# Kernel tuning notes

Measured on AMD Instinct MI355X. Metric: run time of the kernel, lower is better.

## Reference

```python
import jax, jax.numpy as jnp
import numpy as np

D_MODEL = 1024
NUM_HEADS = 16
HEAD_DIM = D_MODEL // NUM_HEADS
HIDDEN = 4096
EPS = 1e-10


def _layernorm(x, gamma, beta):
    mean = jnp.mean(x, axis=-1, keepdims=True)
    var = jnp.var(x, axis=-1, keepdims=True)  # unbiased=False
    return gamma * (x - mean) / jnp.sqrt(var + EPS) + beta


def setup_inputs() -> dict:
    key = jax.random.key(0)
    ks = jax.random.split(key, 16)
    s = 0.02
    d, h = D_MODEL, HIDDEN
    inp = {
        "x": jax.random.normal(ks[0], (4, 2048, d), dtype=jnp.float32),
        "Wq": jax.random.normal(ks[1], (d, d), dtype=jnp.float32) * s,
        "bq": jnp.zeros((d,), jnp.float32),
        "Wk": jax.random.normal(ks[2], (d, d), dtype=jnp.float32) * s,
        "bk": jnp.zeros((d,), jnp.float32),
        "Wv": jax.random.normal(ks[3], (d, d), dtype=jnp.float32) * s,
        "bv": jnp.zeros((d,), jnp.float32),
        "Wo": jax.random.normal(ks[4], (d, d), dtype=jnp.float32) * s,
        "bo": jnp.zeros((d,), jnp.float32),
        "W1": jax.random.normal(ks[5], (d, h), dtype=jnp.float32) * s,
        "b1": jnp.zeros((h,), jnp.float32),
        "W2": jax.random.normal(ks[6], (h, d), dtype=jnp.float32) * s,
        "b2": jnp.zeros((d,), jnp.float32),
        "gamma1": jnp.ones((d,), jnp.float32),
        "beta1": jnp.zeros((d,), jnp.float32),
        "gamma2": jnp.ones((d,), jnp.float32),
        "beta2": jnp.zeros((d,), jnp.float32),
    }
    return inp


def reference(x, Wq, bq, Wk, bk, Wv, bv, Wo, bo, W1, b1, W2, b2,
              gamma1, beta1, gamma2, beta2):
    B, S, D = x.shape
    H, hd = NUM_HEADS, HEAD_DIM
    scale = jnp.sqrt(jnp.float32(hd))

    # --- sublayer 1: self-attention on norm(x), residual add ---
    xn = _layernorm(x, gamma1, beta1)
    Q = (xn @ Wq + bq).reshape(B, S, H, hd).transpose(0, 2, 1, 3)  # [B,H,S,hd]
    K = (xn @ Wk + bk).reshape(B, S, H, hd).transpose(0, 2, 1, 3)
    V = (xn @ Wv + bv).reshape(B, S, H, hd).transpose(0, 2, 1, 3)
    scores = jnp.einsum("bhqd,bhkd->bhqk", Q, K) / scale  # [B,H,S,S]
    attn = jax.nn.softmax(scores, axis=-1)
    ctx = jnp.einsum("bhqk,bhkd->bhqd", attn, V)  # [B,H,S,hd]
    ctx = ctx.transpose(0, 2, 1, 3).reshape(B, S, D)
    x = x + (ctx @ Wo + bo)

    # --- sublayer 2: FFN on norm(x), residual add ---
    xn = _layernorm(x, gamma2, beta2)
    h = jax.nn.gelu(xn @ W1 + b1, approximate=False)  # torch F.gelu default = erf
    x = x + (h @ W2 + b2)
    return x
```

## Files before the change

### kernel.cpp

```cpp
#include <hip/hip_runtime.h>
#include <stdint.h>

#define D_MODEL 1024
#define HIDDEN  4096
#define SEQ     2048
#define NTOK    8192
#define NHEAD   16
#define HDIM    64

typedef unsigned short u16;
typedef __attribute__((ext_vector_type(8))) __bf16 bf16x8;
typedef __attribute__((ext_vector_type(4))) float f32x4;

__device__ __forceinline__ u16 f2bf(float f) {
  union { float f; unsigned u; } c; c.f = f;
  unsigned u = c.u + 0x7fffu + ((c.u >> 16) & 1u);
  return (u16)(u >> 16);
}

__device__ __forceinline__ void gload16(const void* g, void* l) {
  __builtin_amdgcn_global_load_lds((const __attribute__((address_space(1))) void*)g,
                                   (__attribute__((address_space(3))) void*)l, 16, 0, 0);
}

__global__ void transpose_cvt(const float* __restrict__ W, u16* __restrict__ Wt, int K, int N) {
  __shared__ float t[32][33];
  const int k0 = blockIdx.y * 32, n0 = blockIdx.x * 32;
  const int tx = threadIdx.x, ty = threadIdx.y;
#pragma unroll
  for (int p = 0; p < 4; ++p)
    t[ty + p * 8][tx] = W[(size_t)(k0 + ty + p * 8) * N + n0 + tx];
  __syncthreads();
#pragma unroll
  for (int p = 0; p < 4; ++p) {
    const int n = ty + p * 8;
    Wt[(size_t)(n0 + n) * K + k0 + tx] = f2bf(t[tx][n]);
  }
}

__global__ __launch_bounds__(256)
void ln_kernel(const float* __restrict__ x, const float* __restrict__ gamma,
               const float* __restrict__ beta, u16* __restrict__ out) {
  const int row = blockIdx.x;
  const int tid = threadIdx.x;
  const float4 v = ((const float4*)(x + (size_t)row * D_MODEL))[tid];
  float s = v.x + v.y + v.z + v.w;
  float q = v.x * v.x + v.y * v.y + v.z * v.z + v.w * v.w;
#pragma unroll
  for (int o = 32; o > 0; o >>= 1) { s += __shfl_down(s, o); q += __shfl_down(q, o); }
  __shared__ float ps[4], pq[4];
  const int wid = tid >> 6, lane = tid & 63;
  if (lane == 0) { ps[wid] = s; pq[wid] = q; }
  __syncthreads();
  s = ps[0] + ps[1] + ps[2] + ps[3];
  q = pq[0] + pq[1] + pq[2] + pq[3];
  const float mean = s * (1.0f / D_MODEL);
  const float var = q * (1.0f / D_MODEL) - mean * mean;
  const float rstd = rsqrtf(var + 1e-10f);
  const float4 gv = ((const float4*)gamma)[tid];
  const float4 bv = ((const float4*)beta)[tid];
  ushort4 o4;
  o4.x = f2bf((v.x - mean) * rstd * gv.x + bv.x);
  o4.y = f2bf((v.y - mean) * rstd * gv.y + bv.y);
  o4.z = f2bf((v.z - mean) * rstd * gv.z + bv.z);
  o4.w = f2bf((v.w - mean) * rstd * gv.w + bv.w);
  ((ushort4*)(out + (size_t)row * D_MODEL))[tid] = o4;
}

#define SLOT_AE (256 * 32)
#define SLOT_BE (128 * 32)
#define SLOT_E  (SLOT_AE + SLOT_BE)
#define SLOT_BYTES (SLOT_E * 2)

template <int EPI, int KPY, int KPX>
__global__ __launch_bounds__(512, 4)
void gemm32(const u16* __restrict__ A, const u16* __restrict__ Bt,
            const float* __restrict__ bias, const float* __restrict__ res,
            void* __restrict__ outp, int M, int N, int K) {
  __shared__ u16 Ls[3 * SLOT_E];
  const int tid = threadIdx.x;
  const int wid = tid >> 6, lane = tid & 63;
  const int g = lane >> 4, lr = lane & 15;
  const int wr = wid >> 1, wc = wid & 1;

  const int xcd = blockIdx.x & 7, l = blockIdx.x >> 3;
  int bx, by;
  if (KPY > 0) { by = xcd * KPY + (l % KPY); bx = l / KPY; }
  else         { bx = xcd * KPX + (l % KPX); by = l / KPX; }
  const int m0 = by * 256, n0 = bx * 128;

  const int NT = K >> 5;

  const int rA0 = tid >> 2, cc0 = ((tid & 3) ^ (rA0 & 3)) << 3;
  const int u1 = tid + 512;
  const int rA1 = u1 >> 2, cc1 = (((u1 & 3) ^ (rA1 & 3))) << 3;
  const u16* pA0 = A + (size_t)(m0 + rA0) * K + cc0;
  const u16* pA1 = A + (size_t)(m0 + rA1) * K + cc1;
  const u16* pB0 = Bt + (size_t)(n0 + rA0) * K + cc0;
  const int dA0 = wid * 1024;
  const int dA1 = wid * 1024 + 8192;
  const int dB0 = SLOT_AE * 2 + wid * 1024;

  auto stage = [&](int slot) {
    char* sb = (char*)Ls + slot * SLOT_BYTES;
    gload16(pA0, sb + dA0);
    gload16(pA1, sb + dA1);
    gload16(pB0, sb + dB0);
    pA0 += 32; pA1 += 32; pB0 += 32;
  };

  stage(0); stage(1); stage(2);

  f32x4 acc[4][4] = {};
  const int cx = (g ^ (lr & 3)) << 3;

  for (int t = 0; t < NT; ++t) {
    if (t + 3 <= NT)      asm volatile("s_waitcnt vmcnt(6)" ::: "memory");
    else if (t + 2 <= NT) asm volatile("s_waitcnt vmcnt(3)" ::: "memory");
    else                  asm volatile("s_waitcnt vmcnt(0)" ::: "memory");
    asm volatile("s_barrier" ::: "memory");

    const int slot = t % 3;
    const u16* sA = Ls + slot * SLOT_E;
    const u16* sB = sA + SLOT_AE;
    bf16x8 af[4], bfr[4];
#pragma unroll
    for (int mf = 0; mf < 4; ++mf)
      af[mf] = *(const bf16x8*)(sA + (wr * 64 + mf * 16 + lr) * 32 + cx);
#pragma unroll
    for (int nf = 0; nf < 4; ++nf)
      bfr[nf] = *(const bf16x8*)(sB + (wc * 64 + nf * 16 + lr) * 32 + cx);

    __builtin_amdgcn_s_setprio(1);
#pragma unroll
    for (int mf = 0; mf < 4; ++mf)
#pragma unroll
      for (int nf = 0; nf < 4; ++nf)
        acc[mf][nf] = __builtin_amdgcn_mfma_f32_16x16x32_bf16(af[mf], bfr[nf], acc[mf][nf], 0, 0, 0);
    __builtin_amdgcn_s_setprio(0);

    if (t + 3 < NT) {
      asm volatile("s_barrier" ::: "memory");
      stage(slot);
    }
  }

#pragma unroll
  for (int mf = 0; mf < 4; ++mf)
#pragma unroll
    for (int nf = 0; nf < 4; ++nf) {
      const int gn = n0 + wc * 64 + nf * 16 + lr;
      const int gm = m0 + wr * 64 + mf * 16 + 4 * g;
      const float bv = (EPI == 3) ? 0.f : bias[gn];
      const int gn_p = (EPI == 3) ? ((gn & ~63) | ((gn & 15) << 2) | ((gn >> 4) & 3)) : gn;
#pragma unroll
      for (int r = 0; r < 4; ++r) {
        const size_t idx = (size_t)(gm + r) * N + gn_p;
        if (EPI == 0) {
          ((u16*)outp)[idx] = f2bf(acc[mf][nf][r] + bv);
        } else if (EPI == 1) {
          ((float*)outp)[idx] = acc[mf][nf][r] + bv + res[idx];
        } else if (EPI == 2) {
          const float v = acc[mf][nf][r] + bv;
          ((u16*)outp)[idx] = f2bf(0.5f * v * (1.0f + erff(v * 0.7071067811865475f)));
        } else if (EPI == 3) {
          ((u16*)outp)[idx] = f2bf(acc[mf][nf][r] + bias[gm + r]);
        } else {
          ((u16*)outp)[idx] = f2bf((acc[mf][nf][r] + bv) * 0.125f);
        }
      }
    }
}

__global__ __launch_bounds__(256, 4)
void attn_kernel(const u16* __restrict__ Q, const u16* __restrict__ K,
                 const u16* __restrict__ Vt, u16* __restrict__ ctxo) {
  const int bh = blockIdx.y;
  const int b = bh >> 4, h = bh & 15;
  const int q0 = blockIdx.x * 128;
  const int tid = threadIdx.x, wid = tid >> 6, lane = tid & 63;
  const int g = lane >> 4, lr = lane & 15;
  const size_t base = ((size_t)b * SEQ) * D_MODEL + h * HDIM;
  const size_t vbase = ((size_t)h * HDIM) * NTOK + (size_t)b * SEQ;

  __shared__ u16 Ks[64 * 72];
  __shared__ u16 Vts[64 * 72];
  __shared__ u16 Ps[128 * 72];

  const int qw = wid * 32;

#pragma unroll
  for (int i = 0; i < 4; ++i) {
    const int ch = tid + 256 * i, row = ch >> 3, j = ch & 7;
    *(bf16x8*)(Ps + row * 72 + j * 8) =
        *(const bf16x8*)(Q + base + (size_t)(q0 + row) * D_MODEL + j * 8);
  }
  __syncthreads();
  bf16x8 aq[2][2];
#pragma unroll
  for (int qf = 0; qf < 2; ++qf)
#pragma unroll
    for (int ks = 0; ks < 2; ++ks)
      aq[qf][ks] = *(const bf16x8*)(Ps + (qw + qf * 16 + lr) * 72 + ks * 32 + g * 8);

  f32x4 o[2][4] = {};
  float lrun[2][4] = {};

  for (int kv0 = 0; kv0 < SEQ; kv0 += 64) {
    __syncthreads();
#pragma unroll
    for (int i = 0; i < 2; ++i) {
      const int row = (tid >> 3) + i * 32, j = tid & 7;
      *(bf16x8*)(Ks + row * 72 + j * 8) =
          *(const bf16x8*)(K + base + (size_t)(kv0 + row) * D_MODEL + j * 8);
      *(bf16x8*)(Vts + row * 72 + j * 8) =
          *(const bf16x8*)(Vt + vbase + (size_t)row * NTOK + kv0 + j * 8);
    }
    __syncthreads();

    f32x4 s[2][4] = {};
    __builtin_amdgcn_s_setprio(1);
#pragma unroll
    for (int ks = 0; ks < 2; ++ks)
#pragma unroll
      for (int kf = 0; kf < 4; ++kf) {
        const bf16x8 bk = *(const bf16x8*)(Ks + (kf * 16 + lr) * 72 + ks * 32 + g * 8);
#pragma unroll
        for (int qf = 0; qf < 2; ++qf)
          s[qf][kf] = __builtin_amdgcn_mfma_f32_16x16x32_bf16(aq[qf][ks], bk, s[qf][kf], 0, 0, 0);
      }
    __builtin_amdgcn_s_setprio(0);

#pragma unroll
    for (int qf = 0; qf < 2; ++qf)
#pragma unroll
      for (int r = 0; r < 4; ++r) {
        union { float f; unsigned u; } p0, p1, p2, p3;
        p0.f = __expf(s[qf][0][r]);
        p1.f = __expf(s[qf][1][r]);
        p2.f = __expf(s[qf][2][r]);
        p3.f = __expf(s[qf][3][r]);
        lrun[qf][r] += (p0.f + p1.f) + (p2.f + p3.f);
        const unsigned lo = __builtin_amdgcn_perm(p1.u + 0x8000u, p0.u + 0x8000u, 0x07060302u);
        const unsigned hi = __builtin_amdgcn_perm(p3.u + 0x8000u, p2.u + 0x8000u, 0x07060302u);
        *(uint2*)(Ps + (qw + qf * 16 + 4 * g + r) * 72 + lr * 4) = make_uint2(lo, hi);
      }
    asm volatile("s_waitcnt lgkmcnt(0)" ::: "memory");

    __builtin_amdgcn_s_setprio(1);
#pragma unroll
    for (int ks = 0; ks < 2; ++ks) {
      bf16x8 pf[2];
#pragma unroll
      for (int qf = 0; qf < 2; ++qf)
        pf[qf] = *(const bf16x8*)(Ps + (qw + qf * 16 + lr) * 72 + ks * 32 + g * 8);
#pragma unroll
      for (int df = 0; df < 4; ++df) {
        const bf16x8 vf = *(const bf16x8*)(Vts + (df * 16 + lr) * 72 + ks * 32 + g * 8);
#pragma unroll
        for (int qf = 0; qf < 2; ++qf)
          o[qf][df] = __builtin_amdgcn_mfma_f32_16x16x32_bf16(pf[qf], vf, o[qf][df], 0, 0, 0);
      }
    }
    __builtin_amdgcn_s_setprio(0);
  }

#pragma unroll
  for (int off = 1; off < 16; off <<= 1)
#pragma unroll
    for (int qf = 0; qf < 2; ++qf)
#pragma unroll
      for (int r = 0; r < 4; ++r)
        lrun[qf][r] += __shfl_xor(lrun[qf][r], off);

#pragma unroll
  for (int qf = 0; qf < 2; ++qf)
#pragma unroll
    for (int r = 0; r < 4; ++r) {
      const float rinv = 1.0f / lrun[qf][r];
      const int qrow = q0 + qw + qf * 16 + 4 * g + r;
#pragma unroll
      for (int df = 0; df < 4; ++df)
        ctxo[base + (size_t)qrow * D_MODEL + df * 16 + lr] = f2bf(o[qf][df][r] * rinv);
    }
}

extern "C" void kernel_launch(void* const* d_in, const int* in_sizes, int n_in,
                              void* d_out, int out_size, void* d_ws, size_t ws_size,
                              hipStream_t stream) {
  const float* x  = (const float*)d_in[0];
  const float* Wq = (const float*)d_in[1];
  const float* bq = (const float*)d_in[2];
  const float* Wk = (const float*)d_in[3];
  const float* bk = (const float*)d_in[4];
  const float* Wv = (const float*)d_in[5];
  const float* bv = (const float*)d_in[6];
  const float* Wo = (const float*)d_in[7];
  const float* bo = (const float*)d_in[8];
  const float* W1 = (const float*)d_in[9];
  const float* b1 = (const float*)d_in[10];
  const float* W2 = (const float*)d_in[11];
  const float* b2 = (const float*)d_in[12];
  const float* gamma1 = (const float*)d_in[13];
  const float* beta1  = (const float*)d_in[14];
  const float* gamma2 = (const float*)d_in[15];
  const float* beta2  = (const float*)d_in[16];
  float* out = (float*)d_out;

  const size_t M1 = 1u << 20;
  u16* w   = (u16*)d_ws;
  u16* WtQ = w;
  u16* WtK = w + 1 * M1;
  u16* WtV = w + 2 * M1;
  u16* WtO = w + 3 * M1;
  u16* Wt1 = w + 4 * M1;
  u16* Wt2 = w + 8 * M1;
  u16* xn  = w + 12 * M1;
  u16* Qb  = w + 20 * M1;
  u16* Kb  = w + 28 * M1;
  u16* Vtb = w + 36 * M1;
  u16* ctx = w + 44 * M1;
  u16* hb  = w + 20 * M1;
  float* x1 = (float*)(w + 52 * M1);

  const dim3 tb(32, 8);
  transpose_cvt<<<dim3(D_MODEL / 32, D_MODEL / 32), tb, 0, stream>>>(Wq, WtQ, D_MODEL, D_MODEL);
  transpose_cvt<<<dim3(D_MODEL / 32, D_MODEL / 32), tb, 0, stream>>>(Wk, WtK, D_MODEL, D_MODEL);
  transpose_cvt<<<dim3(D_MODEL / 32, D_MODEL / 32), tb, 0, stream>>>(Wv, WtV, D_MODEL, D_MODEL);
  transpose_cvt<<<dim3(D_MODEL / 32, D_MODEL / 32), tb, 0, stream>>>(Wo, WtO, D_MODEL, D_MODEL);
  transpose_cvt<<<dim3(HIDDEN / 32, D_MODEL / 32), tb, 0, stream>>>(W1, Wt1, D_MODEL, HIDDEN);
  transpose_cvt<<<dim3(D_MODEL / 32, HIDDEN / 32), tb, 0, stream>>>(W2, Wt2, HIDDEN, D_MODEL);

  ln_kernel<<<NTOK, 256, 0, stream>>>(x, gamma1, beta1, xn);

  gemm32<4, 4, 0><<<8 * 32, 512, 0, stream>>>(xn, WtQ, bq, nullptr, Qb, NTOK, D_MODEL, D_MODEL);
  gemm32<0, 4, 0><<<8 * 32, 512, 0, stream>>>(xn, WtK, bk, nullptr, Kb, NTOK, D_MODEL, D_MODEL);
  gemm32<3, 0, 8><<<64 * 4, 512, 0, stream>>>(WtV, xn, bv, nullptr, Vtb, D_MODEL, NTOK, D_MODEL);

  attn_kernel<<<dim3(SEQ / 128, 64), 256, 0, stream>>>(Qb, Kb, Vtb, ctx);

  gemm32<1, 4, 0><<<8 * 32, 512, 0, stream>>>(ctx, WtO, bo, x, x1, NTOK, D_MODEL, D_MODEL);

  ln_kernel<<<NTOK, 256, 0, stream>>>(x1, gamma2, beta2, xn);

  gemm32<2, 4, 0><<<32 * 32, 512, 0, stream>>>(xn, Wt1, b1, nullptr, hb, NTOK, HIDDEN, D_MODEL);
  gemm32<1, 4, 0><<<8 * 32, 512, 0, stream>>>(hb, Wt2, b2, x1, out, NTOK, D_MODEL, HIDDEN);
}
```

Baseline: 410.7 us.

## Fuse Q/K projection GEMMs and double attention query tile per block

The Q and K projections now run as a single GEMM with N=2048. Its epilogue routes the left half, with the 0.125 scale, to Q and the right half to K, each with its own bias. This removes one launch and reuses the shared A tiles, but it relies on WtQ and WtK sitting back to back in the workspace. The attention kernel now handles 256 query rows per block as two 128-row sub-tiles that share each loaded K/V tile, which halves K/V global and LDS staging traffic. The cost is more registers per thread, so occupancy drops to 2 blocks per SIMD.

```diff
diff --git a/kernel.cpp b/kernel.cpp
--- a/kernel.cpp
+++ b/kernel.cpp
@@ -75,8 +75,9 @@
 template <int EPI, int KPY, int KPX>
 __global__ __launch_bounds__(512, 4)
 void gemm32(const u16* __restrict__ A, const u16* __restrict__ Bt,
-            const float* __restrict__ bias, const float* __restrict__ res,
-            void* __restrict__ outp, int M, int N, int K) {
+            const float* __restrict__ bias, const float* __restrict__ bias2,
+            const float* __restrict__ res, void* __restrict__ outp, void* __restrict__ outp2,
+            int M, int N, int K) {
   __shared__ u16 Ls[3 * SLOT_E];
   const int tid = threadIdx.x;
   const int wid = tid >> 6, lane = tid & 63;
@@ -151,33 +152,38 @@
     for (int nf = 0; nf < 4; ++nf) {
       const int gn = n0 + wc * 64 + nf * 16 + lr;
       const int gm = m0 + wr * 64 + mf * 16 + 4 * g;
-      const float bv = (EPI == 3) ? 0.f : bias[gn];
-      const int gn_p = (EPI == 3) ? ((gn & ~63) | ((gn & 15) << 2) | ((gn >> 4) & 3)) : gn;
 #pragma unroll
       for (int r = 0; r < 4; ++r) {
-        const size_t idx = (size_t)(gm + r) * N + gn_p;
+        const float av = acc[mf][nf][r];
         if (EPI == 0) {
-          ((u16*)outp)[idx] = f2bf(acc[mf][nf][r] + bv);
+          ((u16*)outp)[(size_t)(gm + r) * N + gn] = f2bf(av + bias[gn]);
         } else if (EPI == 1) {
-          ((float*)outp)[idx] = acc[mf][nf][r] + bv + res[idx];
+          const size_t idx = (size_t)(gm + r) * N + gn;
+          ((float*)outp)[idx] = av + bias[gn] + res[idx];
         } else if (EPI == 2) {
-          const float v = acc[mf][nf][r] + bv;
-          ((u16*)outp)[idx] = f2bf(0.5f * v * (1.0f + erff(v * 0.7071067811865475f)));
+          const float v = av + bias[gn];
+          ((u16*)outp)[(size_t)(gm + r) * N + gn] =
+              f2bf(0.5f * v * (1.0f + erff(v * 0.7071067811865475f)));
         } else if (EPI == 3) {
-          ((u16*)outp)[idx] = f2bf(acc[mf][nf][r] + bias[gm + r]);
+          const int gn_p = (gn & ~63) | ((gn & 15) << 2) | ((gn >> 4) & 3);
+          ((u16*)outp)[(size_t)(gm + r) * N + gn_p] = f2bf(av + bias[gm + r]);
         } else {
-          ((u16*)outp)[idx] = f2bf((acc[mf][nf][r] + bv) * 0.125f);
+          const int side = gn >> 10, col = gn & 1023;
+          u16* o = (u16*)(side ? outp2 : outp);
+          float t_ = av + (side ? bias2[col] : bias[col]);
+          if (!side) t_ *= 0.125f;
+          o[(size_t)(gm + r) * 1024 + col] = f2bf(t_);
         }
       }
     }
 }
 
-__global__ __launch_bounds__(256, 4)
+__global__ __launch_bounds__(256, 2)
 void attn_kernel(const u16* __restrict__ Q, const u16* __restrict__ K,
                  const u16* __restrict__ Vt, u16* __restrict__ ctxo) {
   const int bh = blockIdx.y;
   const int b = bh >> 4, h = bh & 15;
-  const int q0 = blockIdx.x * 128;
+  const int q0 = blockIdx.x * 256;
   const int tid = threadIdx.x, wid = tid >> 6, lane = tid & 63;
   const int g = lane >> 4, lr = lane & 15;
   const size_t base = ((size_t)b * SEQ) * D_MODEL + h * HDIM;
@@ -189,22 +195,26 @@
 
   const int qw = wid * 32;
 
-#pragma unroll
-  for (int i = 0; i < 4; ++i) {
-    const int ch = tid + 256 * i, row = ch >> 3, j = ch & 7;
-    *(bf16x8*)(Ps + row * 72 + j * 8) =
-        *(const bf16x8*)(Q + base + (size_t)(q0 + row) * D_MODEL + j * 8);
+  bf16x8 aq[2][2][2];
+#pragma unroll
+  for (int qt = 0; qt < 2; ++qt) {
+    __syncthreads();
+#pragma unroll
+    for (int i = 0; i < 4; ++i) {
+      const int ch = tid + 256 * i, row = ch >> 3, j = ch & 7;
+      *(bf16x8*)(Ps + row * 72 + j * 8) =
+          *(const bf16x8*)(Q + base + (size_t)(q0 + qt * 128 + row) * D_MODEL + j * 8);
+    }
+    __syncthreads();
+#pragma unroll
+    for (int qf = 0; qf < 2; ++qf)
+#pragma unroll
+      for (int ks = 0; ks < 2; ++ks)
+        aq[qt][qf][ks] = *(const bf16x8*)(Ps + (qw + qf * 16 + lr) * 72 + ks * 32 + g * 8);
   }
-  __syncthreads();
-  bf16x8 aq[2][2];
-#pragma unroll
-  for (int qf = 0; qf < 2; ++qf)
-#pragma unroll
-    for (int ks = 0; ks < 2; ++ks)
-      aq[qf][ks] = *(const bf16x8*)(Ps + (qw + qf * 16 + lr) * 72 + ks * 32 + g * 8);
-
-  f32x4 o[2][4] = {};
-  float lrun[2][4] = {};
+
+  f32x4 o[2][2][4] = {};
+  float lrun[2][2][4] = {};
 
   for (int kv0 = 0; kv0 < SEQ; kv0 += 64) {
     __syncthreads();
@@ -218,71 +228,80 @@
     }
     __syncthreads();
 
-    f32x4 s[2][4] = {};
-    __builtin_amdgcn_s_setprio(1);
-#pragma unroll
-    for (int ks = 0; ks < 2; ++ks)
-#pragma unroll
-      for (int kf = 0; kf < 4; ++kf) {
-        const bf16x8 bk = *(const bf16x8*)(Ks + (kf * 16 + lr) * 72 + ks * 32 + g * 8);
+#pragma unroll
+    for (int qt = 0; qt < 2; ++qt) {
+      f32x4 s[2][4] = {};
+      __builtin_amdgcn_s_setprio(1);
+#pragma unroll
+      for (int ks = 0; ks < 2; ++ks)
+#pragma unroll
+        for (int kf = 0; kf < 4; ++kf) {
+          const bf16x8 bk = *(const bf16x8*)(Ks + (kf * 16 + lr) * 72 + ks * 32 + g * 8);
+#pragma unroll
+          for (int qf = 0; qf < 2; ++qf)
+            s[qf][kf] =
+                __builtin_amdgcn_mfma_f32_16x16x32_bf16(aq[qt][qf][ks], bk, s[qf][kf], 0, 0, 0);
+        }
+      __builtin_amdgcn_s_setprio(0);
+
+#pragma unroll
+      for (int qf = 0; qf < 2; ++qf)
+#pragma unroll
+        for (int r = 0; r < 4; ++r) {
+          union { float f; unsigned u; } p0, p1, p2, p3;
+          p0.f = __expf(s[qf][0][r]);
+          p1.f = __expf(s[qf][1][r]);
+          p2.f = __expf(s[qf][2][r]);
+          p3.f = __expf(s[qf][3][r]);
+          lrun[qt][qf][r] += (p0.f + p1.f) + (p2.f + p3.f);
+          const unsigned lo = __builtin_amdgcn_perm(p1.u + 0x8000u, p0.u + 0x8000u, 0x07060302u);
+          const unsigned hi = __builtin_amdgcn_perm(p3.u + 0x8000u, p2.u + 0x8000u, 0x07060302u);
+          *(uint2*)(Ps + (qw + qf * 16 + 4 * g + r) * 72 + lr * 4) = make_uint2(lo, hi);
+        }
+      asm volatile("s_waitcnt lgkmcnt(0)" ::: "memory");
+
+      __builtin_amdgcn_s_setprio(1);
+#pragma unroll
+      for (int ks = 0; ks < 2; ++ks) {
+        bf16x8 pf[2];
 #pragma unroll
         for (int qf = 0; qf < 2; ++qf)
-          s[qf][kf] = __builtin_amdgcn_mfma_f32_16x16x32_bf16(aq[qf][ks], bk, s[qf][kf], 0, 0, 0);
+          pf[qf] = *(const bf16x8*)(Ps + (qw + qf * 16 + lr) * 72 + ks * 32 + g * 8);
+#pragma unroll
+        for (int df = 0; df < 4; ++df) {
+          const bf16x8 vf = *(const bf16x8*)(Vts + (df * 16 + lr) * 72 + ks * 32 + g * 8);
+#pragma unroll
+          for (int qf = 0; qf < 2; ++qf)
+            o[qt][qf][df] =
+                __builtin_amdgcn_mfma_f32_16x16x32_bf16(pf[qf], vf, o[qt][qf][df], 0, 0, 0);
+        }
       }
-    __builtin_amdgcn_s_setprio(0);
-
+      __builtin_amdgcn_s_setprio(0);
+    }
+  }
+
+#pragma unroll
+  for (int off = 1; off < 16; off <<= 1)
+#pragma unroll
+    for (int qt = 0; qt < 2; ++qt)
+#pragma unroll
+      for (int qf = 0; qf < 2; ++qf)
+#pragma unroll
+        for (int r = 0; r < 4; ++r)
+          lrun[qt][qf][r] += __shfl_xor(lrun[qt][qf][r], off);
+
+#pragma unroll
+  for (int qt = 0; qt < 2; ++qt)
 #pragma unroll
     for (int qf = 0; qf < 2; ++qf)
 #pragma unroll
       for (int r = 0; r < 4; ++r) {
-        union { float f; unsigned u; } p0, p1, p2, p3;
-        p0.f = __expf(s[qf][0][r]);
-        p1.f = __expf(s[qf][1][r]);
-        p2.f = __expf(s[qf][2][r]);
-        p3.f = __expf(s[qf][3][r]);
-        lrun[qf][r] += (p0.f + p1.f) + (p2.f + p3.f);
-        const unsigned lo = __builtin_amdgcn_perm(p1.u + 0x8000u, p0.u + 0x8000u, 0x07060302u);
-        const unsigned hi = __builtin_amdgcn_perm(p3.u + 0x8000u, p2.u + 0x8000u, 0x07060302u);
-        *(uint2*)(Ps + (qw + qf * 16 + 4 * g + r) * 72 + lr * 4) = make_uint2(lo, hi);
+        const float rinv = 1.0f / lrun[qt][qf][r];
+        const int qrow = q0 + qt * 128 + qw + qf * 16 + 4 * g + r;
+#pragma unroll
+        for (int df = 0; df < 4; ++df)
+          ctxo[base + (size_t)qrow * D_MODEL + df * 16 + lr] = f2bf(o[qt][qf][df][r] * rinv);
       }
-    asm volatile("s_waitcnt lgkmcnt(0)" ::: "memory");
-
-    __builtin_amdgcn_s_setprio(1);
-#pragma unroll
-    for (int ks = 0; ks < 2; ++ks) {
-      bf16x8 pf[2];
-#pragma unroll
-      for (int qf = 0; qf < 2; ++qf)
-        pf[qf] = *(const bf16x8*)(Ps + (qw + qf * 16 + lr) * 72 + ks * 32 + g * 8);
-#pragma unroll
-      for (int df = 0; df < 4; ++df) {
-        const bf16x8 vf = *(const bf16x8*)(Vts + (df * 16 + lr) * 72 + ks * 32 + g * 8);
-#pragma unroll
-        for (int qf = 0; qf < 2; ++qf)
-          o[qf][df] = __builtin_amdgcn_mfma_f32_16x16x32_bf16(pf[qf], vf, o[qf][df], 0, 0, 0);
-      }
-    }
-    __builtin_amdgcn_s_setprio(0);
-  }
-
-#pragma unroll
-  for (int off = 1; off < 16; off <<= 1)
-#pragma unroll
-    for (int qf = 0; qf < 2; ++qf)
-#pragma unroll
-      for (int r = 0; r < 4; ++r)
-        lrun[qf][r] += __shfl_xor(lrun[qf][r], off);
-
-#pragma unroll
-  for (int qf = 0; qf < 2; ++qf)
-#pragma unroll
-    for (int r = 0; r < 4; ++r) {
-      const float rinv = 1.0f / lrun[qf][r];
-      const int qrow = q0 + qw + qf * 16 + 4 * g + r;
-#pragma unroll
-      for (int df = 0; df < 4; ++df)
-        ctxo[base + (size_t)qrow * D_MODEL + df * 16 + lr] = f2bf(o[qf][df][r] * rinv);
-    }
 }
 
 extern "C" void kernel_launch(void* const* d_in, const int* in_sizes, int n_in,
@@ -333,16 +352,20 @@
 
   ln_kernel<<<NTOK, 256, 0, stream>>>(x, gamma1, beta1, xn);
 
-  gemm32<4, 4, 0><<<8 * 32, 512, 0, stream>>>(xn, WtQ, bq, nullptr, Qb, NTOK, D_MODEL, D_MODEL);
-  gemm32<0, 4, 0><<<8 * 32, 512, 0, stream>>>(xn, WtK, bk, nullptr, Kb, NTOK, D_MODEL, D_MODEL);
-  gemm32<3, 0, 8><<<64 * 4, 512, 0, stream>>>(WtV, xn, bv, nullptr, Vtb, D_MODEL, NTOK, D_MODEL);
-
-  attn_kernel<<<dim3(SEQ / 128, 64), 256, 0, stream>>>(Qb, Kb, Vtb, ctx);
-
-  gemm32<1, 4, 0><<<8 * 32, 512, 0, stream>>>(ctx, WtO, bo, x, x1, NTOK, D_MODEL, D_MODEL);
+  gemm32<6, 4, 0><<<512, 512, 0, stream>>>(xn, WtQ, bq, bk, nullptr, Qb, Kb,
+                                           NTOK, 2048, D_MODEL);
+  gemm32<3, 0, 8><<<256, 512, 0, stream>>>(WtV, xn, bv, nullptr, nullptr, Vtb, nullptr,
+                                           D_MODEL, NTOK, D_MODEL);
+
+  attn_kernel<<<dim3(SEQ / 256, 64), 256, 0, stream>>>(Qb, Kb, Vtb, ctx);
+
+  gemm32<1, 4, 0><<<256, 512, 0, stream>>>(ctx, WtO, bo, nullptr, x, x1, nullptr,
+                                           NTOK, D_MODEL, D_MODEL);
 
   ln_kernel<<<NTOK, 256, 0, stream>>>(x1, gamma2, beta2, xn);
 
-  gemm32<2, 4, 0><<<32 * 32, 512, 0, stream>>>(xn, Wt1, b1, nullptr, hb, NTOK, HIDDEN, D_MODEL);
-  gemm32<1, 4, 0><<<8 * 32, 512, 0, stream>>>(hb, Wt2, b2, x1, out, NTOK, D_MODEL, HIDDEN);
-}
+  gemm32<2, 4, 0><<<1024, 512, 0, stream>>>(xn, Wt1, b1, nullptr, nullptr, hb, nullptr,
+                                            NTOK, HIDDEN, D_MODEL);
+  gemm32<1, 4, 0><<<256, 512, 0, stream>>>(hb, Wt2, b2, nullptr, x1, out, nullptr,
+                                           NTOK, D_MODEL, HIDDEN);
+}
```

New measurement: 407.4 us. About the same (-0.8%).
